# Kernel tuning notes

Measured on AMD Instinct MI355X. Metric: run time of the kernel, lower is better.

## Reference

```python
import jax, jax.numpy as jnp
import numpy as np

B, S, E, F, R, T = 2, 2048, 768, 3072, 4, 128
H = 12  # num_heads
HD = E // H
HID = 128  # lora_mlp_dim


def _lin(key, out_f, in_f):
    bound = 1.0 / np.sqrt(in_f)
    return jax.random.uniform(key, (out_f, in_f), jnp.float32, -bound, bound)


def _bias(key, out_f, in_f):
    bound = 1.0 / np.sqrt(in_f)
    return jax.random.uniform(key, (out_f,), jnp.float32, -bound, bound)


def setup_inputs() -> dict:
    key = jax.random.key(0)
    ks = jax.random.split(key, 20)
    return {
        "src": jax.random.normal(ks[0], (B, S, E), jnp.float32),
        "task_embedding": jax.random.normal(ks[1], (B, S, T), jnp.float32),
        "norm1_w": jnp.ones((E,), jnp.float32),
        "norm2_w": jnp.ones((E,), jnp.float32),
        "in_proj_w": _lin(ks[2], 3 * E, E),      # MHA qkv, bias=False
        "out_proj_w": _lin(ks[3], E, E),          # MHA out, bias=False
        "ffn1_w": _lin(ks[4], F, E), "ffn1_b": _bias(ks[5], F, E),
        "ffn2_w": _lin(ks[6], E, F), "ffn2_b": _bias(ks[7], E, F),
        "hA_w1": _lin(ks[8], HID, T), "hA_b1": _bias(ks[9], HID, T),
        "hA_w2": _lin(ks[10], F * R, HID), "hA_b2": _bias(ks[11], F * R, HID),
        "hB_w1": _lin(ks[12], HID, T), "hB_b1": _bias(ks[13], HID, T),
        "hB_w2": _lin(ks[14], R * E, HID), "hB_b2": _bias(ks[15], R * E, HID),
    }


def _rmsnorm(x, w):
    eps = jnp.finfo(x.dtype).eps
    return x * jax.lax.rsqrt(jnp.mean(x * x, axis=-1, keepdims=True) + eps) * w


def reference(src, task_embedding, norm1_w, norm2_w, in_proj_w, out_proj_w,
              ffn1_w, ffn1_b, ffn2_w, ffn2_b,
              hA_w1, hA_b1, hA_w2, hA_b2, hB_w1, hB_b1, hB_w2, hB_b2):
    # --- self-attention block (pre-RMSNorm) ---
    x = _rmsnorm(src, norm1_w)
    qkv = jnp.einsum('bse,fe->bsf', x, in_proj_w)  # [B,S,3E]
    q, k, v = jnp.split(qkv, 3, axis=-1)
    q = q.reshape(B, S, H, HD).transpose(0, 2, 1, 3)
    k = k.reshape(B, S, H, HD).transpose(0, 2, 1, 3)
    v = v.reshape(B, S, H, HD).transpose(0, 2, 1, 3)
    scores = jnp.einsum('bhqd,bhkd->bhqk', q, k) / jnp.sqrt(jnp.float32(HD))
    attn = jax.nn.softmax(scores, axis=-1)
    ctx = jnp.einsum('bhqk,bhkd->bhqd', attn, v)
    ctx = ctx.transpose(0, 2, 1, 3).reshape(B, S, E)
    attn_out = jnp.einsum('bse,fe->bsf', ctx, out_proj_w)
    src = src + attn_out

    # --- FFN block with per-token hypernetwork LoRA on linear1 ---
    x = _rmsnorm(src, norm2_w)
    # hypernetwork: MLP(task) -> per-token A [F,R], B [R,E]
    hA = jax.nn.relu(jnp.einsum('bst,ht->bsh', task_embedding, hA_w1) + hA_b1)
    A_params = (jnp.einsum('bsh,fh->bsf', hA, hA_w2) + hA_b2).reshape(B, S, F, R)
    hB = jax.nn.relu(jnp.einsum('bst,ht->bsh', task_embedding, hB_w1) + hB_b1)
    B_params = (jnp.einsum('bsh,fh->bsf', hB, hB_w2) + hB_b2).reshape(B, S, R, E)

    base = jnp.einsum('bse,fe->bsf', x, ffn1_w) + ffn1_b  # [B,S,F]
    inter = jnp.einsum('bse,bsre->bsr', x, B_params)       # [B,S,R]
    adapt = jnp.einsum('bsr,bsfr->bsf', inter, A_params)   # [B,S,F]
    h = jax.nn.relu(base + adapt)
    out2 = jnp.einsum('bsf,ef->bse', h, ffn2_w) + ffn2_b
    return src + out2
```

## Files before the change

### kernel.cpp

```cpp
#include <hip/hip_runtime.h>
#include <math.h>

#define NB 2
#define NS 2048
#define NE 768
#define NF 3072
#define NHEAD 12
#define NTOK 4096
#define LDW 1344
#define VTS 2176

typedef __bf16 bf16;
typedef __bf16 bf16x4 __attribute__((ext_vector_type(4)));
typedef __bf16 bf16x8 __attribute__((ext_vector_type(8)));
typedef float  f32x4  __attribute__((ext_vector_type(4)));

__device__ __forceinline__ f32x4 mfma_bf16(bf16x8 a, bf16x8 b, f32x4 c) {
  return __builtin_amdgcn_mfma_f32_16x16x32_bf16(a, b, c, 0, 0, 0);
}

__device__ __forceinline__ float fast_exp2(float x) {
#if __has_builtin(__builtin_amdgcn_exp2f)
  return __builtin_amdgcn_exp2f(x);
#else
  return exp2f(x);
#endif
}

__device__ __forceinline__ void glds16(const void* g, void* l) {
  __builtin_amdgcn_global_load_lds((const __attribute__((address_space(1))) void*)g,
                                   (__attribute__((address_space(3))) void*)l,
                                   16, 0, 0);
}

__device__ __forceinline__ void swz_xy(int& bx, int& by) {
  int gx = gridDim.x;
  int i = by*gx + bx;
  int xcd = i & 7, s = i >> 3;
  int bands = gridDim.y >> 3;
  by = xcd*bands + s / gx;
  bx = s % gx;
}

__global__ void prep_kernel(const float* __restrict__ in_proj, const float* __restrict__ out_proj,
                            const float* __restrict__ ffn1_w, const float* __restrict__ ffn1_b,
                            const float* __restrict__ ffn2_w,
                            const float* __restrict__ hA_w1, const float* __restrict__ hA_b1,
                            const float* __restrict__ hA_w2, const float* __restrict__ hA_b2,
                            const float* __restrict__ hB_w1, const float* __restrict__ hB_b1,
                            const float* __restrict__ hB_w2,
                            const float* __restrict__ task,
                            bf16* __restrict__ Wqkv, bf16* __restrict__ Wo, bf16* __restrict__ W2,
                            bf16* __restrict__ W1ab, float* __restrict__ b1ab,
                            bf16* __restrict__ WBp, bf16* __restrict__ Wc,
                            bf16* __restrict__ task_bf)
{
  __shared__ float tb[64*130];
  int stride = gridDim.x * blockDim.x;
  int t0 = blockIdx.x * blockDim.x + threadIdx.x;
  const float QS = 0.125f * 1.44269504088896f;
  for (int i = t0; i < (2304*768)/4; i += stride) {
    float4 v = ((const float4*)in_proj)[i];
    float sc = (i < (768*768)/4) ? QS : 1.0f;
    *(bf16x4*)(Wqkv + i*4) = (bf16x4){(bf16)(v.x*sc), (bf16)(v.y*sc), (bf16)(v.z*sc), (bf16)(v.w*sc)};
  }
  for (int i = t0; i < (768*768)/4; i += stride) {
    float4 v = ((const float4*)out_proj)[i];
    *(bf16x4*)(Wo + i*4) = (bf16x4){(bf16)v.x, (bf16)v.y, (bf16)v.z, (bf16)v.w};
  }
  for (int i = t0; i < (768*3072)/4; i += stride) {
    float4 v = ((const float4*)ffn2_w)[i];
    *(bf16x4*)(W2 + i*4) = (bf16x4){(bf16)v.x, (bf16)v.y, (bf16)v.z, (bf16)v.w};
  }
  for (int i = t0; i < (NTOK*128)/4; i += stride) {
    float4 v = ((const float4*)task)[i];
    *(bf16x4*)(task_bf + i*4) = (bf16x4){(bf16)v.x, (bf16)v.y, (bf16)v.z, (bf16)v.w};
  }
  for (int i = t0; i < 256*128;  i += stride)
    W1ab[i] = (bf16)(i < 128*128 ? hA_w1[i] : hB_w1[i - 128*128]);
  for (int i = t0; i < 256; i += stride) b1ab[i] = (i < 128) ? hA_b1[i] : hB_b1[i-128];

  for (int j0 = blockIdx.x*64; j0 < 3072; j0 += gridDim.x*64) {
    __syncthreads();
    for (int i = threadIdx.x; i < 64*128; i += 256) {
      int jr = i >> 7, hh = i & 127;
      tb[jr*130 + hh] = hB_w2[(long)(j0 + jr)*128 + hh];
    }
    __syncthreads();
    int r = j0 / 768, e0 = j0 % 768;
    for (int i = threadIdx.x; i < 128*64; i += 256) {
      int hh = i >> 6, jr = i & 63;
      WBp[(long)(r*128 + hh)*768 + e0 + jr] = (bf16)tb[jr*130 + hh];
    }
  }

  for (int f = blockIdx.x; f < 3072; f += gridDim.x) {
    const float* hrow = hA_w2 + (long)f*512;
    bf16* wrow = Wc + (long)f*LDW;
    for (int c = threadIdx.x; c < 768; c += 256) wrow[c] = (bf16)ffn1_w[(long)f*768 + c];
    for (int i = threadIdx.x; i < 512; i += 256) {
      int r = i >> 7, h = i & 127;
      wrow[768 + h*4 + r] = (bf16)hrow[i];
    }
    if (threadIdx.x < 4)        wrow[1280 + threadIdx.x] = (bf16)hA_b2[f*4 + threadIdx.x];
    else if (threadIdx.x == 4)  wrow[1284] = (bf16)ffn1_b[f];
    else if (threadIdx.x < 64)  wrow[1280 + threadIdx.x] = (bf16)0.f;
  }
}

__global__ __launch_bounds__(256) void rmsnorm_k(const float* __restrict__ x,
                                                 const float* __restrict__ w,
                                                 bf16* __restrict__ out, int ld_out)
{
  __shared__ float red[4];
  long t = blockIdx.x;
  const float* xr = x + t*NE;
  float ss = 0.f;
  #pragma unroll
  for (int i = 0; i < 3; i++) { float v = xr[threadIdx.x + i*256]; ss += v*v; }
  #pragma unroll
  for (int d = 1; d < 64; d <<= 1) ss += __shfl_xor(ss, d, 64);
  if ((threadIdx.x & 63) == 0) red[threadIdx.x >> 6] = ss;
  __syncthreads();
  float tot = red[0] + red[1] + red[2] + red[3];
  float scale = rsqrtf(tot * (1.f/768.f) + 1.1920928955078125e-07f);
  #pragma unroll
  for (int i = 0; i < 3; i++) {
    int idx = threadIdx.x + i*256;
    out[t*ld_out + idx] = (bf16)(xr[idx] * scale * w[idx]);
  }
}

template<typename OutT, bool RELU, bool BIAS, bool RES>
__global__ __launch_bounds__(256) void gemm_bt_sw(const bf16* __restrict__ A,
                                                  const bf16* __restrict__ Bm,
                                                  OutT* __restrict__ C,
                                                  const float* __restrict__ bias,
                                                  const float* __restrict__ res,
                                                  int K, int lda, int ldb, int ldc)
{
  __shared__ bf16 As[2][128*32];
  __shared__ bf16 Bs[2][128*32];
  const int tid = threadIdx.x;
  int bx = blockIdx.x, by = blockIdx.y;
  swz_xy(bx, by);
  const int m0 = by * 128;
  const int n0 = bx * 128;
  const int w = tid >> 6, lane = tid & 63;
  const int quad = lane >> 4, l16 = lane & 15;
  const int wy = w >> 1, wx = w & 1;

  f32x4 acc[4][4];
  #pragma unroll
  for (int i = 0; i < 4; i++)
    #pragma unroll
    for (int j = 0; j < 4; j++) acc[i][j] = (f32x4){0.f,0.f,0.f,0.f};

  const int i0 = tid, i1 = tid + 256;
  const int R0 = i0 >> 3, cc0 = (i0 & 7) ^ (R0 & 7), r0 = 2*R0 + (cc0 >> 2), ch0 = (cc0 & 3) * 8;
  const int R1 = i1 >> 3, cc1 = (i1 & 7) ^ (R1 & 7), r1 = 2*R1 + (cc1 >> 2), ch1 = (cc1 & 3) * 8;
  const bf16* pA0 = A  + (long)(m0 + r0)*lda + ch0;
  const bf16* pA1 = A  + (long)(m0 + r1)*lda + ch1;
  const bf16* pB0 = Bm + (long)(n0 + r0)*ldb + ch0;
  const bf16* pB1 = Bm + (long)(n0 + r1)*ldb + ch1;
  auto stage = [&](int buf) {
    glds16(pA0, (void*)(&As[buf][i0*8]));
    glds16(pA1, (void*)(&As[buf][i1*8]));
    glds16(pB0, (void*)(&Bs[buf][i0*8]));
    glds16(pB1, (void*)(&Bs[buf][i1*8]));
    pA0 += 32; pA1 += 32; pB0 += 32; pB1 += 32;
  };

  stage(0);
  __builtin_amdgcn_s_waitcnt(0);
  __syncthreads();

  const int Rh = l16 >> 1;
  const int ppq = ((l16 & 1) << 2) | quad;
  const int jfr = ppq ^ Rh;
  const int nsteps = K >> 5;
  for (int s = 0; s < nsteps; ++s) {
    const int cur = s & 1;
    if (s + 1 < nsteps) stage(cur ^ 1);

    bf16x8 af[4], bfr[4];
    #pragma unroll
    for (int mi = 0; mi < 4; ++mi)
      af[mi] = *(const bf16x8*)(&As[cur][(wy*32 + mi*8 + Rh)*64 + jfr*8]);
    #pragma unroll
    for (int ni = 0; ni < 4; ++ni)
      bfr[ni] = *(const bf16x8*)(&Bs[cur][(wx*32 + ni*8 + Rh)*64 + jfr*8]);
    #pragma unroll
    for (int mi = 0; mi < 4; ++mi)
      #pragma unroll
      for (int ni = 0; ni < 4; ++ni)
        acc[mi][ni] = mfma_bf16(af[mi], bfr[ni], acc[mi][ni]);

    __builtin_amdgcn_s_waitcnt(0);
    __syncthreads();
  }

  #pragma unroll
  for (int mi = 0; mi < 4; ++mi)
    #pragma unroll
    for (int ni = 0; ni < 4; ++ni) {
      int col = n0 + wx*64 + ni*16 + l16;
      #pragma unroll
      for (int r = 0; r < 4; ++r) {
        long row = m0 + wy*64 + mi*16 + quad*4 + r;
        float v = acc[mi][ni][r];
        if (BIAS) v += bias[col];
        if (RES)  v += res[row*ldc + col];
        if (RELU) v = v > 0.f ? v : 0.f;
        C[row*ldc + col] = (OutT)v;
      }
    }
}

template<typename OutT, bool RELU, bool BIAS, bool RES>
__global__ __launch_bounds__(256) void gemm64(const bf16* __restrict__ A,
                                              const bf16* __restrict__ Bm,
                                              OutT* __restrict__ C,
                                              const float* __restrict__ bias,
                                              const float* __restrict__ res,
                                              int K, int lda, int ldb, int ldc)
{
  __shared__ bf16 As[2][64*64];
  __shared__ bf16 Bs[2][64*64];
  const int tid = threadIdx.x;
  int bx = blockIdx.x, by = blockIdx.y;
  swz_xy(bx, by);
  const int m0 = by * 64, n0 = bx * 64;
  const int w = tid >> 6, lane = tid & 63;
  const int quad = lane >> 4, l16 = lane & 15;
  const int wy = w >> 1, wx = w & 1;
  const int sw = l16 & 7;

  f32x4 acc[2][2];
  #pragma unroll
  for (int i = 0; i < 2; i++)
    #pragma unroll
    for (int j = 0; j < 2; j++) acc[i][j] = (f32x4){0.f,0.f,0.f,0.f};

  const int c0 = tid, c1 = tid + 256;
  const int r0 = c0 >> 3, g0 = ((c0 & 7) ^ (r0 & 7)) * 8;
  const int r1 = c1 >> 3, g1 = ((c1 & 7) ^ (r1 & 7)) * 8;
  const bf16* pA0 = A  + (long)(m0 + r0)*lda + g0;
  const bf16* pA1 = A  + (long)(m0 + r1)*lda + g1;
  const bf16* pB0 = Bm + (long)(n0 + r0)*ldb + g0;
  const bf16* pB1 = Bm + (long)(n0 + r1)*ldb + g1;
  auto stage = [&](int buf) {
    glds16(pA0, (void*)(&As[buf][c0*8]));
    glds16(pA1, (void*)(&As[buf][c1*8]));
    glds16(pB0, (void*)(&Bs[buf][c0*8]));
    glds16(pB1, (void*)(&Bs[buf][c1*8]));
    pA0 += 64; pA1 += 64; pB0 += 64; pB1 += 64;
  };

  stage(0);
  __builtin_amdgcn_s_waitcnt(0);
  __syncthreads();

  const int nsteps = K >> 6;
  for (int s = 0; s < nsteps; ++s) {
    const int cur = s & 1;
    if (s + 1 < nsteps) stage(cur ^ 1);

    bf16x8 af[2][2], bfr[2][2];
    #pragma unroll
    for (int mi = 0; mi < 2; ++mi)
      #pragma unroll
      for (int kb = 0; kb < 2; ++kb)
        af[mi][kb] = *(const bf16x8*)(&As[cur][(wy*32 + mi*16 + l16)*64 + (((kb*4 + quad) ^ sw))*8]);
    #pragma unroll
    for (int ni = 0; ni < 2; ++ni)
      #pragma unroll
      for (int kb = 0; kb < 2; ++kb)
        bfr[ni][kb] = *(const bf16x8*)(&Bs[cur][(wx*32 + ni*16 + l16)*64 + (((kb*4 + quad) ^ sw))*8]);
    #pragma unroll
    for (int kb = 0; kb < 2; ++kb)
      #pragma unroll
      for (int mi = 0; mi < 2; ++mi)
        #pragma unroll
        for (int ni = 0; ni < 2; ++ni)
          acc[mi][ni] = mfma_bf16(af[mi][kb], bfr[ni][kb], acc[mi][ni]);

    __builtin_amdgcn_s_waitcnt(0);
    __syncthreads();
  }

  #pragma unroll
  for (int mi = 0; mi < 2; ++mi)
    #pragma unroll
    for (int ni = 0; ni < 2; ++ni) {
      int col = n0 + wx*32 + ni*16 + l16;
      #pragma unroll
      for (int r = 0; r < 4; ++r) {
        long row = m0 + wy*32 + mi*16 + quad*4 + r;
        float v = acc[mi][ni][r];
        if (BIAS) v += bias[col];
        if (RES)  v += res[row*ldc + col];
        if (RELU) v = v > 0.f ? v : 0.f;
        C[row*ldc + col] = (OutT)v;
      }
    }
}

__global__ __launch_bounds__(256) void gemm_qkv64(const bf16* __restrict__ A,
                                                  const bf16* __restrict__ Bm,
                                                  bf16* __restrict__ Qkv,
                                                  bf16* __restrict__ Vt)
{
  __shared__ bf16 As[2][64*64];
  __shared__ bf16 Bs[2][64*64];
  const int tid = threadIdx.x;
  int bx = blockIdx.x, by = blockIdx.y;
  swz_xy(bx, by);
  const int m0 = by * 64, n0 = bx * 64;
  const int w = tid >> 6, lane = tid & 63;
  const int quad = lane >> 4, l16 = lane & 15;
  const int wy = w >> 1, wx = w & 1;
  const int sw = l16 & 7;

  f32x4 acc[2][2];
  #pragma unroll
  for (int i = 0; i < 2; i++)
    #pragma unroll
    for (int j = 0; j < 2; j++) acc[i][j] = (f32x4){0.f,0.f,0.f,0.f};

  const int c0 = tid, c1 = tid + 256;
  const int r0 = c0 >> 3, g0 = ((c0 & 7) ^ (r0 & 7)) * 8;
  const int r1 = c1 >> 3, g1 = ((c1 & 7) ^ (r1 & 7)) * 8;
  const bf16* pA0 = A  + (long)(m0 + r0)*768 + g0;
  const bf16* pA1 = A  + (long)(m0 + r1)*768 + g1;
  const bf16* pB0 = Bm + (long)(n0 + r0)*768 + g0;
  const bf16* pB1 = Bm + (long)(n0 + r1)*768 + g1;
  auto stage = [&](int buf) {
    glds16(pA0, (void*)(&As[buf][c0*8]));
    glds16(pA1, (void*)(&As[buf][c1*8]));
    glds16(pB0, (void*)(&Bs[buf][c0*8]));
    glds16(pB1, (void*)(&Bs[buf][c1*8]));
    pA0 += 64; pA1 += 64; pB0 += 64; pB1 += 64;
  };

  stage(0);
  __builtin_amdgcn_s_waitcnt(0);
  __syncthreads();

  for (int s = 0; s < 12; ++s) {
    const int cur = s & 1;
    if (s + 1 < 12) stage(cur ^ 1);

    bf16x8 af[2][2], bfr[2][2];
    #pragma unroll
    for (int mi = 0; mi < 2; ++mi)
      #pragma unroll
      for (int kb = 0; kb < 2; ++kb)
        af[mi][kb] = *(const bf16x8*)(&As[cur][(wy*32 + mi*16 + l16)*64 + (((kb*4 + quad) ^ sw))*8]);
    #pragma unroll
    for (int ni = 0; ni < 2; ++ni)
      #pragma unroll
      for (int kb = 0; kb < 2; ++kb)
        bfr[ni][kb] = *(const bf16x8*)(&Bs[cur][(wx*32 + ni*16 + l16)*64 + (((kb*4 + quad) ^ sw))*8]);
    #pragma unroll
    for (int kb = 0; kb < 2; ++kb)
      #pragma unroll
      for (int mi = 0; mi < 2; ++mi)
        #pragma unroll
        for (int ni = 0; ni < 2; ++ni)
          acc[mi][ni] = mfma_bf16(af[mi][kb], bfr[ni][kb], acc[mi][ni]);

    __builtin_amdgcn_s_waitcnt(0);
    __syncthreads();
  }

  const int bb = m0 >> 11;
  #pragma unroll
  for (int mi = 0; mi < 2; ++mi)
    #pragma unroll
    for (int ni = 0; ni < 2; ++ni) {
      int col = n0 + wx*32 + ni*16 + l16;
      #pragma unroll
      for (int r = 0; r < 4; ++r) {
        long row = m0 + wy*32 + mi*16 + quad*4 + r;
        bf16 v = (bf16)acc[mi][ni][r];
        if (col < 1536) {
          Qkv[row*2304 + col] = v;
        } else {
          int vc = col - 1536;
          int hh = vc >> 6, d = vc & 63;
          long srow = row & (NS-1);
          Vt[((long)(bb*NHEAD + hh)*64 + d)*VTS + srow] = v;
        }
      }
    }
}

__global__ __launch_bounds__(256, 2) void flash_attn(const bf16* __restrict__ Qkv,
                                                     const bf16* __restrict__ Vt,
                                                     bf16* __restrict__ Ctx)
{
  __shared__ bf16 Ks[2][2][64*64];
  __shared__ bf16 Vs[2][2][64*64];

  const int tid = threadIdx.x;
  const int w = tid >> 6, lane = tid & 63;
  const int quad = lane >> 4, l16 = lane & 15;
  const int pair = w >> 1, qw = w & 1;
  int bx = blockIdx.x, by = blockIdx.y;
  swz_xy(bx, by);
  const int bh = by;
  const int b = bh / NHEAD, h = bh % NHEAD;
  const int q0 = bx * 64;

  bf16x8 qf[2][2];
  #pragma unroll
  for (int mi = 0; mi < 2; ++mi) {
    const long tq = (long)(b*NS + q0 + qw*32 + mi*16 + l16);
    qf[mi][0] = *(const bf16x8*)(Qkv + tq*2304 + h*64 + quad*8);
    qf[mi][1] = *(const bf16x8*)(Qkv + tq*2304 + h*64 + 32 + quad*8);
  }

  bf16x8 ones;
  #pragma unroll
  for (int j = 0; j < 8; ++j) ones[j] = (bf16)1.0f;

  f32x4 o[2][4];
  f32x4 o5[2];
  #pragma unroll
  for (int mi = 0; mi < 2; ++mi) {
    o5[mi] = (f32x4){0.f,0.f,0.f,0.f};
    #pragma unroll
    for (int i = 0; i < 4; i++) o[mi][i] = (f32x4){0.f,0.f,0.f,0.f};
  }

  const int ptid = tid & 127;
  const bf16* kp[4];
  const bf16* vp[4];
  int cc[4];
  #pragma unroll
  for (int i = 0; i < 4; ++i) {
    int c = ptid + i*128;
    cc[i] = c;
    int r = c >> 3, g = ((c & 7) ^ (r & 7)) * 8;
    kp[i] = Qkv + (long)(b*NS + pair*1024 + r)*2304 + 768 + h*64 + g;
    vp[i] = Vt + ((long)bh*64 + r)*VTS + pair*1024 + g;
  }
  auto stage = [&](int buf) {
    #pragma unroll
    for (int i = 0; i < 4; ++i) {
      glds16(kp[i], (void*)(&Ks[pair][buf][cc[i]*8]));
      glds16(vp[i], (void*)(&Vs[pair][buf][cc[i]*8]));
      kp[i] += (long)64*2304; vp[i] += 64;
    }
  };

  auto body = [&](int cur) {
    bf16x8 kfr[4][2];
    #pragma unroll
    for (int nt = 0; nt < 4; ++nt)
      #pragma unroll
      for (int kb = 0; kb < 2; ++kb)
        kfr[nt][kb] = *(const bf16x8*)(&Ks[pair][cur][(nt*16 + l16)*64 + (((kb*4 + quad) ^ (l16 & 7)))*8]);

    bf16x8 pf[2][2];
    #pragma unroll
    for (int mi = 0; mi < 2; ++mi) {
      f32x4 s[4];
      #pragma unroll
      for (int nt = 0; nt < 4; ++nt) {
        s[nt] = (f32x4){0.f,0.f,0.f,0.f};
        #pragma unroll
        for (int kb = 0; kb < 2; ++kb)
          s[nt] = mfma_bf16(kfr[nt][kb], qf[mi][kb], s[nt]);
      }
      #pragma unroll
      for (int nt = 0; nt < 4; ++nt)
        #pragma unroll
        for (int r = 0; r < 4; ++r)
          pf[mi][nt >> 1][(nt & 1)*4 + r] = (bf16)fast_exp2(s[nt][r]);
    }
    #pragma unroll
    for (int ntp = 0; ntp < 2; ++ntp) {
      bf16x8 vf[4];
      #pragma unroll
      for (int dt = 0; dt < 4; ++dt) {
        int row = dt*16 + l16;
        int cA = ntp*4 + (quad >> 1);
        int base = row*64 + (quad & 1)*4;
        bf16x4 va = *(const bf16x4*)(&Vs[pair][cur][base + ((cA       ^ (row & 7)) << 3)]);
        bf16x4 vb = *(const bf16x4*)(&Vs[pair][cur][base + (((cA + 2) ^ (row & 7)) << 3)]);
        vf[dt] = (bf16x8){va[0],va[1],va[2],va[3], vb[0],vb[1],vb[2],vb[3]};
      }
      #pragma unroll
      for (int mi = 0; mi < 2; ++mi) {
        #pragma unroll
        for (int dt = 0; dt < 4; ++dt)
          o[mi][dt] = mfma_bf16(pf[mi][ntp], vf[dt], o[mi][dt]);
        o5[mi] = mfma_bf16(pf[mi][ntp], ones, o5[mi]);
      }
    }
  };

  stage(0);
  __builtin_amdgcn_s_waitcnt(0);
  __syncthreads();

  for (int t = 0; t < 16; t += 2) {
    stage(1);
    body(0);
    __builtin_amdgcn_s_waitcnt(0);
    __syncthreads();
    if (t + 2 < 16) stage(0);
    body(1);
    __builtin_amdgcn_s_waitcnt(0);
    __syncthreads();
  }

  float* Of = (float*)&Ks[0][0][0];
  float* Lf = Of + 64*68;
  const int rbase = qw*32;
  if (pair == 1) {
    #pragma unroll
    for (int mi = 0; mi < 2; ++mi)
      #pragma unroll
      for (int r = 0; r < 4; ++r) {
        int row = rbase + mi*16 + quad*4 + r;
        if (l16 == 0) Lf[row] = o5[mi][r];
        #pragma unroll
        for (int dt = 0; dt < 4; ++dt)
          Of[row*68 + dt*16 + l16] = o[mi][dt][r];
      }
  }
  __syncthreads();
  if (pair == 0) {
    #pragma unroll
    for (int mi = 0; mi < 2; ++mi)
      #pragma unroll
      for (int r = 0; r < 4; ++r) {
        int row = rbase + mi*16 + quad*4 + r;
        float inv = 1.f / (o5[mi][r] + Lf[row]);
        long trow = (long)(b*NS + q0 + row);
        #pragma unroll
        for (int dt = 0; dt < 4; ++dt)
          Ctx[trow*NE + h*64 + dt*16 + l16] =
            (bf16)((o[mi][dt][r] + Of[row*68 + dt*16 + l16]) * inv);
      }
  }
}

__global__ __launch_bounds__(256) void build_g(const bf16* __restrict__ HAB,
                                               const float* __restrict__ P,
                                               const float* __restrict__ hB_b2,
                                               bf16* __restrict__ Aext)
{
  long t = blockIdx.x*4 + (threadIdx.x >> 6);
  int lane = threadIdx.x & 63;
  const bf16* xr = Aext + t*LDW;
  float acc[4] = {0.f, 0.f, 0.f, 0.f};
  for (int i = lane; i < 768; i += 64) {
    float xv = (float)xr[i];
    #pragma unroll
    for (int r = 0; r < 4; ++r) acc[r] += xv * hB_b2[r*768 + i];
  }
  const bf16* hB = HAB + t*256 + 128;
  const float* Pr = P + t*512;
  #pragma unroll
  for (int k = 0; k < 2; ++k) {
    int h = lane + k*64;
    float hv = (float)hB[h];
    #pragma unroll
    for (int r = 0; r < 4; ++r) acc[r] += hv * Pr[r*128 + h];
  }
  #pragma unroll
  for (int r = 0; r < 4; ++r)
    #pragma unroll
    for (int d = 1; d < 64; d <<= 1) acc[r] += __shfl_xor(acc[r], d, 64);

  bf16* grow = Aext + t*LDW + 768;
  const bf16* hA = HAB + t*256;
  #pragma unroll
  for (int j = 0; j < 8; ++j) {
    int idx = lane*8 + j;
    int h = idx >> 2, r = idx & 3;
    grow[idx] = (bf16)((float)hA[h] * acc[r]);
  }
  if (lane < 4)       Aext[t*LDW + 1280 + lane] = (bf16)acc[lane];
  else if (lane == 4) Aext[t*LDW + 1284] = (bf16)1.0f;
  else                Aext[t*LDW + 1280 + lane] = (bf16)0.f;
}

extern "C" void kernel_launch(void* const* d_in, const int* in_sizes, int n_in,
                              void* d_out, int out_size, void* d_ws, size_t ws_size,
                              hipStream_t stream)
{
  const float* src      = (const float*)d_in[0];
  const float* task     = (const float*)d_in[1];
  const float* norm1_w  = (const float*)d_in[2];
  const float* norm2_w  = (const float*)d_in[3];
  const float* in_proj  = (const float*)d_in[4];
  const float* out_proj = (const float*)d_in[5];
  const float* ffn1_w   = (const float*)d_in[6];
  const float* ffn1_b   = (const float*)d_in[7];
  const float* ffn2_w   = (const float*)d_in[8];
  const float* ffn2_b   = (const float*)d_in[9];
  const float* hA_w1    = (const float*)d_in[10];
  const float* hA_b1    = (const float*)d_in[11];
  const float* hA_w2    = (const float*)d_in[12];
  const float* hA_b2    = (const float*)d_in[13];
  const float* hB_w1    = (const float*)d_in[14];
  const float* hB_b1    = (const float*)d_in[15];
  const float* hB_w2    = (const float*)d_in[16];
  const float* hB_b2    = (const float*)d_in[17];
  float* out = (float*)d_out;

  char* ws = (char*)d_ws;
  size_t off = 0;
  auto alloc = [&](size_t bytes) { size_t o = off; off += (bytes + 255) & ~(size_t)255; return o; };
  bf16*  Wqkv   = (bf16*)(ws + alloc(2304*768*2));
  bf16*  Wo     = (bf16*)(ws + alloc(768*768*2));
  bf16*  W2     = (bf16*)(ws + alloc(768*3072*2));
  bf16*  W1ab   = (bf16*)(ws + alloc(256*128*2));
  float* b1ab   = (float*)(ws + alloc(256*4));
  bf16*  WBp    = (bf16*)(ws + alloc(512*768*2));
  bf16*  Wc     = (bf16*)(ws + alloc((size_t)3072*LDW*2));
  bf16*  taskbf = (bf16*)(ws + alloc((size_t)NTOK*128*2));
  bf16*  XC     = (bf16*)(ws + alloc((size_t)NTOK*768*2));
  char*  QKVH   = ws + alloc(25559040);
  bf16*  Qkv    = (bf16*)QKVH;
  bf16*  Vt     = (bf16*)(QKVH + 18874368);
  bf16*  Hbuf   = (bf16*)QKVH;
  float* Src2   = (float*)(ws + alloc((size_t)NTOK*768*4));
  bf16*  Aext   = (bf16*)(ws + alloc((size_t)NTOK*LDW*2));
  bf16*  HAB    = (bf16*)(ws + alloc((size_t)NTOK*256*2));
  float* P      = (float*)(ws + alloc((size_t)NTOK*512*4));

  prep_kernel<<<dim3(1280), 256, 0, stream>>>(in_proj, out_proj, ffn1_w, ffn1_b, ffn2_w,
      hA_w1, hA_b1, hA_w2, hA_b2, hB_w1, hB_b1, hB_w2, task,
      Wqkv, Wo, W2, W1ab, b1ab, WBp, Wc, taskbf);
  rmsnorm_k<<<dim3(NTOK), 256, 0, stream>>>(src, norm1_w, XC, 768);
  gemm_qkv64<<<dim3(36,64), 256, 0, stream>>>(XC, Wqkv, Qkv, Vt);
  flash_attn<<<dim3(32,24), 256, 0, stream>>>(Qkv, Vt, XC);
  gemm64<float,false,false,true><<<dim3(12,64), 256, 0, stream>>>(XC, Wo, Src2, nullptr, src, 768, 768, 768, 768);
  rmsnorm_k<<<dim3(NTOK), 256, 0, stream>>>(Src2, norm2_w, Aext, LDW);
  gemm64<bf16,true,true,false><<<dim3(4,64), 256, 0, stream>>>(taskbf, W1ab, HAB, b1ab, nullptr, 128, 128, 128, 256);
  gemm64<float,false,false,false><<<dim3(8,64), 256, 0, stream>>>(Aext, WBp, P, nullptr, nullptr, 768, LDW, 768, 512);
  build_g<<<dim3(NTOK/4), 256, 0, stream>>>(HAB, P, hB_b2, Aext);
  gemm_bt_sw<bf16,true,false,false><<<dim3(24,32), 256, 0, stream>>>(Aext, Wc, Hbuf, nullptr, nullptr, 1312, LDW, LDW, 3072);
  gemm64<float,false,true,true><<<dim3(12,64), 256, 0, stream>>>(Hbuf, W2, out, ffn2_b, Src2, 3072, 3072, 3072, 768);
}
```

Before: 212.4 us.

## Triple-buffer GEMM shared-memory tiles with partial vmcnt waits

Converts the double-buffered global-to-LDS staging in the three GEMM kernels into a three-stage ring. The loop now waits only until the oldest stage has landed (vmcnt(4)) instead of draining all loads, so two tile loads stay in flight during compute. This is meant to hide global load latency behind MFMA work. It costs 50% more LDS per block, which may lower occupancy. Correctness relies on exactly four outstanding loads per stage.

```diff
diff --git a/kernel.cpp b/kernel.cpp
--- a/kernel.cpp
+++ b/kernel.cpp
@@ -31,6 +31,17 @@
   __builtin_amdgcn_global_load_lds((const __attribute__((address_space(1))) void*)g,
                                    (__attribute__((address_space(3))) void*)l,
                                    16, 0, 0);
+}
+
+__device__ __forceinline__ void pipe_barrier_keep4() {
+  asm volatile("s_waitcnt vmcnt(4)" ::: "memory");
+  __builtin_amdgcn_s_barrier();
+  __builtin_amdgcn_sched_barrier(0);
+}
+__device__ __forceinline__ void pipe_barrier_drain() {
+  asm volatile("s_waitcnt vmcnt(0)" ::: "memory");
+  __builtin_amdgcn_s_barrier();
+  __builtin_amdgcn_sched_barrier(0);
 }
 
 __device__ __forceinline__ void swz_xy(int& bx, int& by) {
@@ -139,8 +150,8 @@
                                                   const float* __restrict__ res,
                                                   int K, int lda, int ldb, int ldc)
 {
-  __shared__ bf16 As[2][128*32];
-  __shared__ bf16 Bs[2][128*32];
+  __shared__ bf16 As[3][128*32];
+  __shared__ bf16 Bs[3][128*32];
   const int tid = threadIdx.x;
   int bx = blockIdx.x, by = blockIdx.y;
   swz_xy(bx, by);
@@ -172,16 +183,17 @@
   };
 
   stage(0);
-  __builtin_amdgcn_s_waitcnt(0);
-  __syncthreads();
+  stage(1);
+  pipe_barrier_keep4();
 
   const int Rh = l16 >> 1;
   const int ppq = ((l16 & 1) << 2) | quad;
   const int jfr = ppq ^ Rh;
   const int nsteps = K >> 5;
+  int cur = 0, nx2 = 2;
   for (int s = 0; s < nsteps; ++s) {
-    const int cur = s & 1;
-    if (s + 1 < nsteps) stage(cur ^ 1);
+    const bool more = (s + 2 < nsteps);
+    if (more) stage(nx2);
 
     bf16x8 af[4], bfr[4];
     #pragma unroll
@@ -196,8 +208,10 @@
       for (int ni = 0; ni < 4; ++ni)
         acc[mi][ni] = mfma_bf16(af[mi], bfr[ni], acc[mi][ni]);
 
-    __builtin_amdgcn_s_waitcnt(0);
-    __syncthreads();
+    if (more) pipe_barrier_keep4();
+    else      pipe_barrier_drain();
+    cur = (cur == 2) ? 0 : cur + 1;
+    nx2 = (nx2 == 2) ? 0 : nx2 + 1;
   }
 
   #pragma unroll
@@ -225,8 +239,8 @@
                                               const float* __restrict__ res,
                                               int K, int lda, int ldb, int ldc)
 {
-  __shared__ bf16 As[2][64*64];
-  __shared__ bf16 Bs[2][64*64];
+  __shared__ bf16 As[3][64*64];
+  __shared__ bf16 Bs[3][64*64];
   const int tid = threadIdx.x;
   int bx = blockIdx.x, by = blockIdx.y;
   swz_xy(bx, by);
@@ -257,14 +271,15 @@
     pA0 += 64; pA1 += 64; pB0 += 64; pB1 += 64;
   };
 
+  const int nsteps = K >> 6;
   stage(0);
-  __builtin_amdgcn_s_waitcnt(0);
-  __syncthreads();
-
-  const int nsteps = K >> 6;
+  if (nsteps > 1) stage(1);
+  pipe_barrier_keep4();
+
+  int cur = 0, nx2 = 2;
   for (int s = 0; s < nsteps; ++s) {
-    const int cur = s & 1;
-    if (s + 1 < nsteps) stage(cur ^ 1);
+    const bool more = (s + 2 < nsteps);
+    if (more) stage(nx2);
 
     bf16x8 af[2][2], bfr[2][2];
     #pragma unroll
@@ -285,8 +300,10 @@
         for (int ni = 0; ni < 2; ++ni)
           acc[mi][ni] = mfma_bf16(af[mi][kb], bfr[ni][kb], acc[mi][ni]);
 
-    __builtin_amdgcn_s_waitcnt(0);
-    __syncthreads();
+    if (more) pipe_barrier_keep4();
+    else      pipe_barrier_drain();
+    cur = (cur == 2) ? 0 : cur + 1;
+    nx2 = (nx2 == 2) ? 0 : nx2 + 1;
   }
 
   #pragma unroll
@@ -311,8 +328,8 @@
                                                   bf16* __restrict__ Qkv,
                                                   bf16* __restrict__ Vt)
 {
-  __shared__ bf16 As[2][64*64];
-  __shared__ bf16 Bs[2][64*64];
+  __shared__ bf16 As[3][64*64];
+  __shared__ bf16 Bs[3][64*64];
   const int tid = threadIdx.x;
   int bx = blockIdx.x, by = blockIdx.y;
   swz_xy(bx, by);
@@ -344,12 +361,13 @@
   };
 
   stage(0);
-  __builtin_amdgcn_s_waitcnt(0);
-  __syncthreads();
-
+  stage(1);
+  pipe_barrier_keep4();
+
+  int cur = 0, nx2 = 2;
   for (int s = 0; s < 12; ++s) {
-    const int cur = s & 1;
-    if (s + 1 < 12) stage(cur ^ 1);
+    const bool more = (s + 2 < 12);
+    if (more) stage(nx2);
 
     bf16x8 af[2][2], bfr[2][2];
     #pragma unroll
@@ -370,8 +388,10 @@
         for (int ni = 0; ni < 2; ++ni)
           acc[mi][ni] = mfma_bf16(af[mi][kb], bfr[ni][kb], acc[mi][ni]);
 
-    __builtin_amdgcn_s_waitcnt(0);
-    __syncthreads();
+    if (more) pipe_barrier_keep4();
+    else      pipe_barrier_drain();
+    cur = (cur == 2) ? 0 : cur + 1;
+    nx2 = (nx2 == 2) ? 0 : nx2 + 1;
   }
 
   const int bb = m0 >> 11;
```

Result: no change. 212.5 us (+0.1%).
